# Kernel tuning notes

Measured on AMD Instinct MI355X. Metric: run time of the kernel, lower is better.

Reference implementation:

```python
import jax, jax.numpy as jnp
import numpy as np

D = 1024  # dim_model

def setup_inputs() -> dict:
    key = jax.random.key(0)
    ks = jax.random.split(key, 7)
    s = 1.0 / np.sqrt(D)
    inputs = jax.random.normal(ks[0], (4, 2048, D), dtype=jnp.float32)
    Wq = jax.random.uniform(ks[1], (D, D), jnp.float32, -s, s)
    bq = jax.random.uniform(ks[2], (D,), jnp.float32, -s, s)
    Wk = jax.random.uniform(ks[3], (D, D), jnp.float32, -s, s)
    bk = jax.random.uniform(ks[4], (D,), jnp.float32, -s, s)
    Wv = jax.random.uniform(ks[5], (D, D), jnp.float32, -s, s)
    bv = jax.random.uniform(ks[6], (D,), jnp.float32, -s, s)
    return {"inputs": inputs, "Wq": Wq, "bq": bq, "Wk": Wk, "bk": bk, "Wv": Wv, "bv": bv}

def reference(inputs, Wq, bq, Wk, bk, Wv, bv):
    # torch Linear: y = x @ W.T + b
    q = jnp.einsum('bsd,ed->bse', inputs, Wq) + bq  # [B,S,D]
    k = jnp.einsum('bsd,ed->bse', inputs, Wk) + bk
    v = jnp.einsum('bsd,ed->bse', inputs, Wv) + bv
    scale = 1.0 / jnp.sqrt(jnp.float32(inputs.shape[-1]))
    scores = jnp.einsum('bqd,bkd->bqk', q, k) * scale  # [B,S,S]
    attn = jax.nn.softmax(scores, axis=-1)
    cross_attended_vision = jnp.einsum('bqk,bkd->bqd', attn, v)
    cross_attended_text = jnp.einsum('bqk,bqd->bkd', attn, inputs)  # attn^T @ inputs
    return (cross_attended_vision, cross_attended_text)
```

## Files before the change

kernel.cpp:

```cpp
#include <hip/hip_runtime.h>
#include <hip/hip_bf16.h>
#include <stdint.h>

typedef unsigned short u16;
typedef u16   us8    __attribute__((ext_vector_type(8)));
typedef __bf16 bf16x8 __attribute__((ext_vector_type(8)));
typedef float f32x4  __attribute__((ext_vector_type(4)));

#define DEV static __device__ __forceinline__

DEV u16 f2bf(float f) {
  uint32_t u = __builtin_bit_cast(uint32_t, f);
  u += 0x7FFFu + ((u >> 16) & 1u);
  return (u16)(u >> 16);
}
DEV float bf2f(u16 s) { return __builtin_bit_cast(float, (uint32_t)s << 16); }

DEV void gl16(const void* g, void* l) {
  __builtin_amdgcn_global_load_lds((const __attribute__((address_space(1))) void*)g,
                                   (__attribute__((address_space(3))) void*)l, 16, 0, 0);
}

__global__ __launch_bounds__(256) void k_cvt_all(
    const float* __restrict__ x, const float* __restrict__ wq,
    const float* __restrict__ wk, const float* __restrict__ wv,
    const float* __restrict__ bq, const float* __restrict__ bk,
    u16* __restrict__ out, float* __restrict__ bQK, int xn4, int wn4) {
  int i = blockIdx.x * 256 + threadIdx.x;
  const int cvt_tot = xn4 + 3 * wn4;
  if (i < cvt_tot) {
    const float* src;
    int idx;
    if (i < xn4) { src = x; idx = i; }
    else {
      int j = i - xn4;
      if (j < wn4) { src = wq; idx = j; }
      else if (j < 2 * wn4) { src = wk; idx = j - wn4; }
      else { src = wv; idx = j - 2 * wn4; }
    }
    float4 v = reinterpret_cast<const float4*>(src)[idx];
    uint2 o;
    o.x = (uint32_t)f2bf(v.x) | ((uint32_t)f2bf(v.y) << 16);
    o.y = (uint32_t)f2bf(v.z) | ((uint32_t)f2bf(v.w) << 16);
    reinterpret_cast<uint2*>(out)[i] = o;
  } else {
    int j = i - cvt_tot;
    if (j < 256)      reinterpret_cast<float4*>(bQK)[j] = reinterpret_cast<const float4*>(bq)[j];
    else if (j < 512) reinterpret_cast<float4*>(bQK)[j] = reinterpret_cast<const float4*>(bk)[j - 256];
  }
}

#define SB0 __builtin_amdgcn_sched_barrier(0)
#define LGKM(N) do { asm volatile("s_waitcnt lgkmcnt(" #N ")" ::: "memory"); \
                     __builtin_amdgcn_sched_barrier(0); } while (0)

template <bool OUT_BF16, int BIAS_MODE>
DEV void gemm_body(const u16* __restrict__ A, const u16* __restrict__ B,
                   void* __restrict__ Cv, const float* __restrict__ bias,
                   int K, int lda, int ldb, int ldc, float alpha,
                   int m0, int n0, long long cbase, u16* AsB, u16* BsB) {
  const int t = threadIdx.x;
  const int lane = t & 63;
  const int wid = t >> 6;
  const int wm = wid >> 2;
  const int wn = wid & 3;
  const int l15 = lane & 15, l4 = lane >> 4;

  const int prow = t >> 3;
  const int scol = ((t & 7) ^ (prow & 7)) * 8;
  const u16* Abase = A + (long long)(m0 + prow) * lda + scol;
  const u16* Bbase = B + (long long)(n0 + prow) * ldb + scol;
  const long long a64 = (long long)64 * lda, a128 = (long long)128 * lda;
  const long long b64 = (long long)64 * ldb, b128 = (long long)128 * ldb;
  u16* AsT = AsB + t * 8;
  u16* BsT = BsB + t * 8;

#define STG_A(h, kt) { const u16* s_ = Abase + (h) * a128 + (long long)(kt) * 64; \
    u16* d_ = AsT + (((kt) & 1) * 2 + (h)) * 8192; gl16(s_, d_); gl16(s_ + a64, d_ + 4096); }
#define STG_B(h, kt) { const u16* s_ = Bbase + (h) * b128 + (long long)(kt) * 64; \
    u16* d_ = BsT + (((kt) & 1) * 2 + (h)) * 8192; gl16(s_, d_); gl16(s_ + b64, d_ + 4096); }

  const int aro = wm * 64 + l15;
  const int bro = wn * 32 + l15;
  const int cs0 = ((l4) ^ (l15 & 7)) * 8;
  const int cs1 = ((4 + l4) ^ (l15 & 7)) * 8;
#define LD(base, row, cs) (*(const bf16x8*)&(base)[(row) * 64 + (cs)])

  f32x4 acc[8][4];
#pragma unroll
  for (int i = 0; i < 8; ++i)
#pragma unroll
    for (int j = 0; j < 4; ++j) { f32x4 z = {0.f, 0.f, 0.f, 0.f}; acc[i][j] = z; }

  const int NT = K >> 6;

  STG_A(0, 0); STG_A(1, 0); STG_B(0, 0); STG_B(1, 0);
  STG_A(0, 1); STG_B(0, 1);
  asm volatile("s_waitcnt vmcnt(4)" ::: "memory");
  __builtin_amdgcn_s_barrier();

#define MK(f_, fn_, k_)                                                         \
  acc[f_][fn_] = __builtin_amdgcn_mfma_f32_16x16x32_bf16(af[f_][k_], bfr[fn_][k_], acc[f_][fn_], 0, 0, 0)
#define M1P(fn_, k_)                                                            \
  acc[4][fn_] = __builtin_amdgcn_mfma_f32_16x16x32_bf16(a1[k_], bfr[fn_][k_], acc[4][fn_], 0, 0, 0)
#define M1(f_, fn_, k_)                                                         \
  acc[4 + (f_)][fn_] = __builtin_amdgcn_mfma_f32_16x16x32_bf16(af1[(f_) - 1][k_], bfr[fn_][k_], acc[4 + (f_)][fn_], 0, 0, 0)

  for (int tt = 0; tt < NT; ++tt) {
    const int p = tt & 1;
    const bool s1 = (tt + 1 < NT);
    const bool s2 = (tt + 2 < NT);
    bf16x8 bfr[4][2];
    bf16x8 a1[2];

    {
      const u16* Ah  = AsB + (p * 2) * 8192;
      const u16* Ah1 = AsB + (p * 2 + 1) * 8192;
      const u16* Bh0 = BsB + (p * 2) * 8192;
      const u16* Bh1 = BsB + (p * 2 + 1) * 8192;
      bf16x8 af[4][2];
      bfr[0][0] = LD(Bh0, bro, cs0);      bfr[0][1] = LD(Bh0, bro, cs1);
      bfr[1][0] = LD(Bh0, bro + 16, cs0); bfr[1][1] = LD(Bh0, bro + 16, cs1);
      af[0][0]  = LD(Ah, aro, cs0);       af[0][1]  = LD(Ah, aro, cs1);
      SB0;
      bfr[2][0] = LD(Bh1, bro, cs0);      bfr[2][1] = LD(Bh1, bro, cs1);
      bfr[3][0] = LD(Bh1, bro + 16, cs0); bfr[3][1] = LD(Bh1, bro + 16, cs1);
      af[1][0]  = LD(Ah, aro + 16, cs0);  af[1][1]  = LD(Ah, aro + 16, cs1);
      SB0;
      af[2][0] = LD(Ah, aro + 32, cs0);   af[2][1] = LD(Ah, aro + 32, cs1);
      SB0;
      af[3][0] = LD(Ah, aro + 48, cs0);   af[3][1] = LD(Ah, aro + 48, cs1);
      if (s1) { STG_A(1, tt + 1); STG_B(1, tt + 1); }
      SB0;
      a1[0] = LD(Ah1, aro, cs0);          a1[1] = LD(Ah1, aro, cs1);
      SB0;
      LGKM(12);
      __builtin_amdgcn_s_setprio(1);
      MK(0, 0, 0); MK(0, 1, 0);
      LGKM(6);
      MK(0, 2, 0); MK(0, 3, 0);
      MK(1, 0, 0); MK(1, 1, 0); MK(1, 2, 0); MK(1, 3, 0);
      LGKM(4);
      MK(2, 0, 0); MK(2, 1, 0); MK(2, 2, 0); MK(2, 3, 0);
      LGKM(2);
      MK(3, 0, 0); MK(3, 1, 0); MK(3, 2, 0); MK(3, 3, 0);
      MK(0, 0, 1); MK(0, 1, 1); MK(0, 2, 1); MK(0, 3, 1);
      MK(1, 0, 1); MK(1, 1, 1); MK(1, 2, 1); MK(1, 3, 1);
      MK(2, 0, 1); MK(2, 1, 1); MK(2, 2, 1); MK(2, 3, 1);
      MK(3, 0, 1); MK(3, 1, 1); MK(3, 2, 1); MK(3, 3, 1);
      __builtin_amdgcn_s_setprio(0);
      __builtin_amdgcn_s_barrier();
    }

    {
      const u16* Ah1 = AsB + (p * 2 + 1) * 8192;
      bf16x8 af1[3][2];
      af1[0][0] = LD(Ah1, aro + 16, cs0); af1[0][1] = LD(Ah1, aro + 16, cs1);
      SB0;
      af1[1][0] = LD(Ah1, aro + 32, cs0); af1[1][1] = LD(Ah1, aro + 32, cs1);
      SB0;
      af1[2][0] = LD(Ah1, aro + 48, cs0); af1[2][1] = LD(Ah1, aro + 48, cs1);
      if (s2) { STG_A(0, tt + 2); STG_B(0, tt + 2); }
      SB0;
      LGKM(6);
      __builtin_amdgcn_s_setprio(1);
      M1P(0, 0); M1P(1, 0); M1P(2, 0); M1P(3, 0);
      LGKM(4);
      M1(1, 0, 0); M1(1, 1, 0); M1(1, 2, 0); M1(1, 3, 0);
      LGKM(2);
      M1(2, 0, 0); M1(2, 1, 0); M1(2, 2, 0); M1(2, 3, 0);
      LGKM(0);
      M1(3, 0, 0); M1(3, 1, 0); M1(3, 2, 0); M1(3, 3, 0);
      M1P(0, 1); M1P(1, 1); M1P(2, 1); M1P(3, 1);
      M1(1, 0, 1); M1(1, 1, 1); M1(1, 2, 1); M1(1, 3, 1);
      M1(2, 0, 1); M1(2, 1, 1); M1(2, 2, 1); M1(2, 3, 1);
      M1(3, 0, 1); M1(3, 1, 1); M1(3, 2, 1); M1(3, 3, 1);
      __builtin_amdgcn_s_setprio(0);
      if (s2) { asm volatile("s_waitcnt vmcnt(4)" ::: "memory"); }
      else    { asm volatile("s_waitcnt vmcnt(0)" ::: "memory"); }
      __builtin_amdgcn_s_barrier();
    }
  }
#undef STG_A
#undef STG_B
#undef MK
#undef M1P
#undef M1
#undef LD

#pragma unroll
  for (int am = 0; am < 8; ++am) {
    const int qm = am >> 2, f = am & 3;
    const int grow0 = m0 + qm * 128 + wm * 64 + f * 16 + l4 * 4;
#pragma unroll
    for (int an = 0; an < 4; ++an) {
      const int gcol = n0 + (an >> 1) * 128 + wn * 32 + (an & 1) * 16 + l15;
      float bc = 0.f;
      if (BIAS_MODE == 1) bc = bias[gcol];
#pragma unroll
      for (int r = 0; r < 4; ++r) {
        float bv_ = (BIAS_MODE == 2) ? bias[grow0 + r] : bc;
        float v = acc[am][an][r] * alpha + bv_;
        long long idx = cbase + (long long)(grow0 + r) * ldc + gcol;
        if constexpr (OUT_BF16) ((u16*)Cv)[idx] = f2bf(v);
        else                    ((float*)Cv)[idx] = v;
      }
    }
  }
}

template <bool OUT_BF16>
__global__ __launch_bounds__(512, 2) void k_gemm8(
    const u16* __restrict__ A, const u16* __restrict__ B,
    void* __restrict__ Cv, int K, int lda, int ldb, int ldc,
    long long sA, long long sB, long long sC, float alpha, int gx, int gy) {
  __shared__ alignas(16) u16 lds[65536];
  const int nwg = gridDim.x;
  int lin = blockIdx.x;
  lin = (lin & 7) * (nwg >> 3) + (lin >> 3);
  const int gxy = gx * gy;
  const int bz = lin / gxy;
  const int rem = lin - bz * gxy;
  const int by = rem / gx;
  const int bx = rem - by * gx;
  gemm_body<OUT_BF16, 0>(A + (long long)bz * sA, B + (long long)bz * sB, Cv,
                         nullptr, K, lda, ldb, ldc, alpha,
                         by * 256, bx * 256, (long long)bz * sC,
                         lds, lds + 32768);
}

__global__ __launch_bounds__(512, 2) void k_projQK(
    const u16* __restrict__ xb, const u16* __restrict__ Wqkv,
    const float* __restrict__ bQK, u16* __restrict__ QKb) {
  __shared__ alignas(16) u16 lds[65536];
  int lin = (blockIdx.x & 7) * 32 + (blockIdx.x >> 3);
  const int by = lin >> 3, bx = lin & 7;
  gemm_body<true, 1>(xb, Wqkv, QKb, bQK, 1024, 1024, 1024, 2048, 1.0f,
                     by * 256, bx * 256, 0, lds, lds + 32768);
}

__global__ __launch_bounds__(512, 2) void k_sv(
    const u16* __restrict__ xb, const u16* __restrict__ Wqkv,
    const float* __restrict__ bv, const u16* __restrict__ QKb,
    u16* __restrict__ P, u16* __restrict__ VTX) {
  __shared__ alignas(16) u16 lds[65536];
  const int bid = blockIdx.x;
  if (bid < 384) {
    int lin = (bid & 7) * 48 + (bid >> 3);
    if (lin < 256) {
      const int z = lin >> 6;
      const int rem = lin & 63;
      const int by = rem >> 3, bx = rem & 7;
      const long long qoff = (long long)z * 2048 * 2048;
      gemm_body<true, 0>(QKb + qoff, QKb + 1024 + qoff, P, nullptr,
                         1024, 2048, 2048, 2048, 0.03125f,
                         by * 256, bx * 256, (long long)z * 2048 * 2048,
                         lds, lds + 32768);
    } else {
      const int l2 = lin - 256;
      const int by = l2 >> 5, bx = l2 & 31;
      gemm_body<true, 2>(Wqkv + 2048 * 1024, xb, VTX, bv, 1024, 1024, 1024,
                         16384, 1.0f, by * 256, bx * 256, 0, lds, lds + 32768);
    }
  } else {
    const int tb = bid - 384;
    const int r0 = (tb >> 4) * 64, c0 = (tb & 15) * 64;
    const int tx = threadIdx.x & 63, ty = threadIdx.x >> 6;
    u16* tile = lds;
#pragma unroll
    for (int i = 0; i < 64; i += 8)
      tile[(ty + i) * 65 + tx] = xb[(long long)(r0 + ty + i) * 1024 + c0 + tx];
    __syncthreads();
#pragma unroll
    for (int i = 0; i < 64; i += 8)
      VTX[(long long)(c0 + ty + i) * 16384 + 8192 + r0 + tx] = tile[tx * 65 + ty + i];
  }
}

__global__ __launch_bounds__(256) void k_softmax(u16* __restrict__ P) {
  const long long row = blockIdx.x;
  u16* p = P + row * 2048;
  const int t = threadIdx.x;
  us8 v = *reinterpret_cast<const us8*>(&p[t * 8]);
  float f[8];
#pragma unroll
  for (int j = 0; j < 8; ++j) f[j] = bf2f(v[j]);
  float m = f[0];
#pragma unroll
  for (int j = 1; j < 8; ++j) m = fmaxf(m, f[j]);
#pragma unroll
  for (int o = 32; o > 0; o >>= 1) m = fmaxf(m, __shfl_xor(m, o));
  __shared__ float redm[4], reds[4];
  if ((t & 63) == 0) redm[t >> 6] = m;
  __syncthreads();
  m = fmaxf(fmaxf(redm[0], redm[1]), fmaxf(redm[2], redm[3]));
  float s = 0.f;
#pragma unroll
  for (int j = 0; j < 8; ++j) {
    f[j] = __expf(f[j] - m);
    s += f[j];
  }
#pragma unroll
  for (int o = 32; o > 0; o >>= 1) s += __shfl_xor(s, o);
  if ((t & 63) == 0) reds[t >> 6] = s;
  __syncthreads();
  s = reds[0] + reds[1] + reds[2] + reds[3];
  const float inv = 1.0f / s;
  us8 o8;
#pragma unroll
  for (int j = 0; j < 8; ++j) o8[j] = f2bf(f[j] * inv);
  *reinterpret_cast<us8*>(&p[t * 8]) = o8;
}

__global__ __launch_bounds__(512) void k_tr64(const u16* __restrict__ in,
                                              u16* __restrict__ out,
                                              int ld, long long sIO) {
  __shared__ u16 tile[64 * 65];
  const long long base = (long long)blockIdx.z * sIO;
  const int r0 = blockIdx.y * 64, c0 = blockIdx.x * 64;
  const int tx = threadIdx.x & 63, ty = threadIdx.x >> 6;
#pragma unroll
  for (int i = 0; i < 64; i += 8)
    tile[(ty + i) * 65 + tx] = in[base + (long long)(r0 + ty + i) * ld + c0 + tx];
  __syncthreads();
#pragma unroll
  for (int i = 0; i < 64; i += 8)
    out[base + (long long)(c0 + ty + i) * ld + r0 + tx] = tile[tx * 65 + ty + i];
}

extern "C" void kernel_launch(void* const* d_in, const int* in_sizes, int n_in,
                              void* d_out, int out_size, void* d_ws, size_t ws_size,
                              hipStream_t stream) {
  (void)in_sizes; (void)n_in; (void)out_size;
  const float* x  = (const float*)d_in[0];
  const float* Wq = (const float*)d_in[1];
  const float* bq = (const float*)d_in[2];
  const float* Wk = (const float*)d_in[3];
  const float* bk = (const float*)d_in[4];
  const float* Wv = (const float*)d_in[5];
  const float* bv = (const float*)d_in[6];
  float* out = (float*)d_out;

  const int B = 4, S = 2048, D = 1024;
  const long long MX = (long long)B * S;

  const long long need = MX * D * 2
                       + 3LL * D * D * 2
                       + 2048 * 4
                       + MX * 2 * D * 2
                       + 2LL * B * S * S * 2
                       + (long long)D * 16384 * 2;
  if ((long long)ws_size < need) return;

  char* w = (char*)d_ws;
  u16*   xb   = (u16*)w;   w += MX * D * 2;
  u16*   Wqkv = (u16*)w;   w += 3LL * D * D * 2;
  float* bQK  = (float*)w; w += 2048 * 4;
  u16*   QKb  = (u16*)w;   w += MX * 2 * D * 2;
  u16*   P    = (u16*)w;   w += (long long)B * S * S * 2;
  u16*   PT   = (u16*)w;   w += (long long)B * S * S * 2;
  u16*   VTX  = (u16*)w;   w += (long long)D * 16384 * 2;
  (void)Wqkv;

  dim3 blk256(256), blk512(512);

  {
    int xn4 = (int)(MX * D / 4);
    int wn4 = D * D / 4;
    int tot = xn4 + 3 * wn4 + 512;
    k_cvt_all<<<dim3((tot + 255) / 256), blk256, 0, stream>>>(
        x, Wq, Wk, Wv, bq, bk, xb, bQK, xn4, wn4);
  }

  k_projQK<<<dim3(256), blk512, 0, stream>>>(xb, Wqkv, bQK, QKb);

  k_sv<<<dim3(384 + 2048), blk512, 0, stream>>>(xb, Wqkv, bv, QKb, P, VTX);

  k_softmax<<<dim3((int)(B * S)), blk256, 0, stream>>>(P);

  k_tr64<<<dim3(32, 32, 4), blk512, 0, stream>>>(P, PT, S, (long long)S * S);

  k_gemm8<false><<<dim3(256), blk512, 0, stream>>>(
      P, VTX, out, S, S, 16384, D,
      (long long)S * S, 2048, (long long)S * D, 1.0f, 4, 8);
}
```

Measured before the change: 196.1 us.

## Fuse softmax exp and transpose into score GEMM epilogue, defer normalization

The score GEMM epilogue now computes exp of the scaled scores without max subtraction, writes both the row-major and transposed bf16 tiles, and emits per-tile partial row sums. A small kernel reduces those sums into inverse normalizers and folds them into the scaled transposed x. The final GEMM applies the row normalizer in its epilogue. This removes the standalone softmax and transpose kernels and one full pass over the score matrix. Without the max subtraction, exp can overflow if scores grow large.

```diff
diff --git a/kernel.cpp b/kernel.cpp
--- a/kernel.cpp
+++ b/kernel.cpp
@@ -4,6 +4,7 @@
 
 typedef unsigned short u16;
 typedef u16   us8    __attribute__((ext_vector_type(8)));
+typedef u16   us4    __attribute__((ext_vector_type(4)));
 typedef __bf16 bf16x8 __attribute__((ext_vector_type(8)));
 typedef float f32x4  __attribute__((ext_vector_type(4)));
 
@@ -188,6 +189,45 @@
 #undef M1
 #undef LD
 
+  if constexpr (BIAS_MODE == 4) {
+    u16* Cb = (u16*)Cv;
+    float* psum = const_cast<float*>(bias);
+    float* lds_ps = (float*)AsB;
+#pragma unroll
+    for (int am = 0; am < 8; ++am) {
+      const int qm = am >> 2, f = am & 3;
+      const int lrow0 = qm * 128 + wm * 64 + f * 16 + l4 * 4;
+      float rp[4] = {0.f, 0.f, 0.f, 0.f};
+#pragma unroll
+      for (int an = 0; an < 4; ++an) {
+        const int gcol = n0 + (an >> 1) * 128 + wn * 32 + (an & 1) * 16 + l15;
+        us4 et;
+#pragma unroll
+        for (int r = 0; r < 4; ++r) {
+          float e = __expf(acc[am][an][r] * alpha);
+          rp[r] += e;
+          u16 h = f2bf(e);
+          Cb[cbase + (long long)(m0 + lrow0 + r) * 2048 + gcol] = h;
+          et[r] = h;
+        }
+        *(us4*)&Cb[cbase + 4LL * 2048 * 2048 + (long long)gcol * 2048 + (m0 + lrow0)] = et;
+      }
+#pragma unroll
+      for (int r = 0; r < 4; ++r) {
+        float v = rp[r];
+        v += __shfl_xor(v, 1); v += __shfl_xor(v, 2);
+        v += __shfl_xor(v, 4); v += __shfl_xor(v, 8);
+        if (l15 == 0) lds_ps[(lrow0 + r) * 4 + wn] = v;
+      }
+    }
+    __syncthreads();
+    if (t < 256) {
+      float s = lds_ps[t * 4] + lds_ps[t * 4 + 1] + lds_ps[t * 4 + 2] + lds_ps[t * 4 + 3];
+      const long long gq = (cbase >> 11) + m0 + t;
+      psum[gq * 8 + (n0 >> 8)] = s;
+    }
+    return;
+  }
 #pragma unroll
   for (int am = 0; am < 8; ++am) {
     const int qm = am >> 2, f = am & 3;
@@ -199,34 +239,16 @@
       if (BIAS_MODE == 1) bc = bias[gcol];
 #pragma unroll
       for (int r = 0; r < 4; ++r) {
-        float bv_ = (BIAS_MODE == 2) ? bias[grow0 + r] : bc;
-        float v = acc[am][an][r] * alpha + bv_;
+        float v = acc[am][an][r] * alpha;
+        if (BIAS_MODE == 1) v += bc;
+        if (BIAS_MODE == 2) v += bias[grow0 + r];
+        if (BIAS_MODE == 3) v *= bias[grow0 + r];
         long long idx = cbase + (long long)(grow0 + r) * ldc + gcol;
         if constexpr (OUT_BF16) ((u16*)Cv)[idx] = f2bf(v);
         else                    ((float*)Cv)[idx] = v;
       }
     }
   }
-}
-
-template <bool OUT_BF16>
-__global__ __launch_bounds__(512, 2) void k_gemm8(
-    const u16* __restrict__ A, const u16* __restrict__ B,
-    void* __restrict__ Cv, int K, int lda, int ldb, int ldc,
-    long long sA, long long sB, long long sC, float alpha, int gx, int gy) {
-  __shared__ alignas(16) u16 lds[65536];
-  const int nwg = gridDim.x;
-  int lin = blockIdx.x;
-  lin = (lin & 7) * (nwg >> 3) + (lin >> 3);
-  const int gxy = gx * gy;
-  const int bz = lin / gxy;
-  const int rem = lin - bz * gxy;
-  const int by = rem / gx;
-  const int bx = rem - by * gx;
-  gemm_body<OUT_BF16, 0>(A + (long long)bz * sA, B + (long long)bz * sB, Cv,
-                         nullptr, K, lda, ldb, ldc, alpha,
-                         by * 256, bx * 256, (long long)bz * sC,
-                         lds, lds + 32768);
 }
 
 __global__ __launch_bounds__(512, 2) void k_projQK(
@@ -239,93 +261,75 @@
                      by * 256, bx * 256, 0, lds, lds + 32768);
 }
 
-__global__ __launch_bounds__(512, 2) void k_sv(
+__global__ __launch_bounds__(512, 2) void k_sc(
     const u16* __restrict__ xb, const u16* __restrict__ Wqkv,
     const float* __restrict__ bv, const u16* __restrict__ QKb,
-    u16* __restrict__ P, u16* __restrict__ VTX) {
+    u16* __restrict__ E, u16* __restrict__ VTX, float* __restrict__ psum) {
   __shared__ alignas(16) u16 lds[65536];
-  const int bid = blockIdx.x;
-  if (bid < 384) {
-    int lin = (bid & 7) * 48 + (bid >> 3);
-    if (lin < 256) {
-      const int z = lin >> 6;
-      const int rem = lin & 63;
-      const int by = rem >> 3, bx = rem & 7;
-      const long long qoff = (long long)z * 2048 * 2048;
-      gemm_body<true, 0>(QKb + qoff, QKb + 1024 + qoff, P, nullptr,
-                         1024, 2048, 2048, 2048, 0.03125f,
-                         by * 256, bx * 256, (long long)z * 2048 * 2048,
-                         lds, lds + 32768);
-    } else {
-      const int l2 = lin - 256;
-      const int by = l2 >> 5, bx = l2 & 31;
-      gemm_body<true, 2>(Wqkv + 2048 * 1024, xb, VTX, bv, 1024, 1024, 1024,
-                         16384, 1.0f, by * 256, bx * 256, 0, lds, lds + 32768);
-    }
+  int lin = (blockIdx.x & 7) * 48 + (blockIdx.x >> 3);
+  if (lin < 256) {
+    const int z = lin >> 6;
+    const int rem = lin & 63;
+    const int by = rem >> 3, bx = rem & 7;
+    const long long qoff = (long long)z * 2048 * 2048;
+    gemm_body<true, 4>(QKb + qoff, QKb + 1024 + qoff, E, (const float*)psum,
+                       1024, 2048, 2048, 2048, 0.03125f,
+                       by * 256, bx * 256, (long long)z * 2048 * 2048,
+                       lds, lds + 32768);
   } else {
-    const int tb = bid - 384;
-    const int r0 = (tb >> 4) * 64, c0 = (tb & 15) * 64;
-    const int tx = threadIdx.x & 63, ty = threadIdx.x >> 6;
-    u16* tile = lds;
-#pragma unroll
-    for (int i = 0; i < 64; i += 8)
-      tile[(ty + i) * 65 + tx] = xb[(long long)(r0 + ty + i) * 1024 + c0 + tx];
-    __syncthreads();
-#pragma unroll
-    for (int i = 0; i < 64; i += 8)
-      VTX[(long long)(c0 + ty + i) * 16384 + 8192 + r0 + tx] = tile[tx * 65 + ty + i];
-  }
-}
-
-__global__ __launch_bounds__(256) void k_softmax(u16* __restrict__ P) {
-  const long long row = blockIdx.x;
-  u16* p = P + row * 2048;
+    const int l2 = lin - 256;
+    const int by = l2 >> 5, bx = l2 & 31;
+    gemm_body<true, 2>(Wqkv + 2048 * 1024, xb, VTX, bv, 1024, 1024, 1024,
+                       16384, 1.0f, by * 256, bx * 256, 0, lds, lds + 32768);
+  }
+}
+
+__global__ __launch_bounds__(256) void k_xt(
+    const u16* __restrict__ xb, const float* __restrict__ psum,
+    float* __restrict__ il_arr, u16* __restrict__ VTX) {
+  __shared__ u16 tile[64 * 65];
+  __shared__ float lds_il[64];
+  const int tb = blockIdx.x;
+  const int r0 = (tb >> 4) * 64;
+  const int c0 = (tb & 15) * 64;
   const int t = threadIdx.x;
-  us8 v = *reinterpret_cast<const us8*>(&p[t * 8]);
-  float f[8];
-#pragma unroll
-  for (int j = 0; j < 8; ++j) f[j] = bf2f(v[j]);
-  float m = f[0];
-#pragma unroll
-  for (int j = 1; j < 8; ++j) m = fmaxf(m, f[j]);
-#pragma unroll
-  for (int o = 32; o > 0; o >>= 1) m = fmaxf(m, __shfl_xor(m, o));
-  __shared__ float redm[4], reds[4];
-  if ((t & 63) == 0) redm[t >> 6] = m;
+  if (t < 64) {
+    const float* pp = psum + (long long)(r0 + t) * 8;
+    float s = pp[0] + pp[1] + pp[2] + pp[3] + pp[4] + pp[5] + pp[6] + pp[7];
+    float iv = 1.0f / s;
+    lds_il[t] = iv;
+    if (c0 == 0) il_arr[r0 + t] = iv;
+  }
   __syncthreads();
-  m = fmaxf(fmaxf(redm[0], redm[1]), fmaxf(redm[2], redm[3]));
-  float s = 0.f;
-#pragma unroll
-  for (int j = 0; j < 8; ++j) {
-    f[j] = __expf(f[j] - m);
-    s += f[j];
-  }
-#pragma unroll
-  for (int o = 32; o > 0; o >>= 1) s += __shfl_xor(s, o);
-  if ((t & 63) == 0) reds[t >> 6] = s;
+  const int tx = t & 63, ty = t >> 6;
+#pragma unroll
+  for (int i = 0; i < 64; i += 4)
+    tile[(ty + i) * 65 + tx] =
+        f2bf(bf2f(xb[(long long)(r0 + ty + i) * 1024 + c0 + tx]) * lds_il[ty + i]);
   __syncthreads();
-  s = reds[0] + reds[1] + reds[2] + reds[3];
-  const float inv = 1.0f / s;
-  us8 o8;
-#pragma unroll
-  for (int j = 0; j < 8; ++j) o8[j] = f2bf(f[j] * inv);
-  *reinterpret_cast<us8*>(&p[t * 8]) = o8;
-}
-
-__global__ __launch_bounds__(512) void k_tr64(const u16* __restrict__ in,
-                                              u16* __restrict__ out,
-                                              int ld, long long sIO) {
-  __shared__ u16 tile[64 * 65];
-  const long long base = (long long)blockIdx.z * sIO;
-  const int r0 = blockIdx.y * 64, c0 = blockIdx.x * 64;
-  const int tx = threadIdx.x & 63, ty = threadIdx.x >> 6;
-#pragma unroll
-  for (int i = 0; i < 64; i += 8)
-    tile[(ty + i) * 65 + tx] = in[base + (long long)(r0 + ty + i) * ld + c0 + tx];
-  __syncthreads();
-#pragma unroll
-  for (int i = 0; i < 64; i += 8)
-    out[base + (long long)(c0 + ty + i) * ld + r0 + tx] = tile[tx * 65 + ty + i];
+#pragma unroll
+  for (int i = 0; i < 64; i += 4)
+    VTX[(long long)(c0 + ty + i) * 16384 + 8192 + r0 + tx] = tile[tx * 65 + ty + i];
+}
+
+__global__ __launch_bounds__(512, 2) void k_out(
+    const u16* __restrict__ E, const u16* __restrict__ VTX,
+    float* __restrict__ out, const float* __restrict__ il) {
+  __shared__ alignas(16) u16 lds[65536];
+  int lin = (blockIdx.x & 7) * 32 + (blockIdx.x >> 3);
+  const int bz = lin >> 5;
+  const int rem = lin & 31;
+  const int by = rem >> 2, bx = rem & 3;
+  if (bz < 4)
+    gemm_body<false, 3>(E + (long long)bz * 2048 * 2048, VTX + (long long)bz * 2048,
+                        out, il + bz * 2048, 2048, 2048, 16384, 1024, 1.0f,
+                        by * 256, bx * 256, (long long)bz * 2048 * 1024,
+                        lds, lds + 32768);
+  else
+    gemm_body<false, 0>(E + (long long)bz * 2048 * 2048, VTX + (long long)bz * 2048,
+                        out, nullptr, 2048, 2048, 16384, 1024, 1.0f,
+                        by * 256, bx * 256, (long long)bz * 2048 * 1024,
+                        lds, lds + 32768);
 }
 
 extern "C" void kernel_launch(void* const* d_in, const int* in_sizes, int n_in,
@@ -349,7 +353,9 @@
                        + 2048 * 4
                        + MX * 2 * D * 2
                        + 2LL * B * S * S * 2
-                       + (long long)D * 16384 * 2;
+                       + (long long)D * 16384 * 2
+                       + MX * 8 * 4
+                       + MX * 4;
   if ((long long)ws_size < need) return;
 
   char* w = (char*)d_ws;
@@ -357,10 +363,12 @@
   u16*   Wqkv = (u16*)w;   w += 3LL * D * D * 2;
   float* bQK  = (float*)w; w += 2048 * 4;
   u16*   QKb  = (u16*)w;   w += MX * 2 * D * 2;
-  u16*   P    = (u16*)w;   w += (long long)B * S * S * 2;
-  u16*   PT   = (u16*)w;   w += (long long)B * S * S * 2;
+  u16*   E    = (u16*)w;   w += (long long)B * S * S * 2;
+  u16*   ET   = (u16*)w;   w += (long long)B * S * S * 2;
   u16*   VTX  = (u16*)w;   w += (long long)D * 16384 * 2;
-  (void)Wqkv;
+  float* psum = (float*)w; w += MX * 8 * 4;
+  float* ilv  = (float*)w; w += MX * 4;
+  (void)Wqkv; (void)ET;
 
   dim3 blk256(256), blk512(512);
 
@@ -374,13 +382,9 @@
 
   k_projQK<<<dim3(256), blk512, 0, stream>>>(xb, Wqkv, bQK, QKb);
 
-  k_sv<<<dim3(384 + 2048), blk512, 0, stream>>>(xb, Wqkv, bv, QKb, P, VTX);
-
-  k_softmax<<<dim3((int)(B * S)), blk256, 0, stream>>>(P);
-
-  k_tr64<<<dim3(32, 32, 4), blk512, 0, stream>>>(P, PT, S, (long long)S * S);
-
-  k_gemm8<false><<<dim3(256), blk512, 0, stream>>>(
-      P, VTX, out, S, S, 16384, D,
-      (long long)S * S, 2048, (long long)S * D, 1.0f, 4, 8);
-}
+  k_sc<<<dim3(384), blk512, 0, stream>>>(xb, Wqkv, bv, QKb, E, VTX, psum);
+
+  k_xt<<<dim3(2048), blk256, 0, stream>>>(xb, psum, ilv, VTX);
+
+  k_out<<<dim3(256), blk512, 0, stream>>>(E, VTX, out, ilv);
+}
```

After: 193.0 us, median of 2. No clear change (-1.6%).
